# Performance work log

Measured on AMD Instinct MI355X. Metric: run time of the kernel, lower is better.

The kernel has to match this reference:

```python
import jax, jax.numpy as jnp
import numpy as np

B, S, D_IN, D_OUT, H = 4, 2048, 2048, 2048, 16
DH = D_OUT // H  # 128


def setup_inputs() -> dict:
    key = jax.random.key(0)
    ks = jax.random.split(key, 6)
    scale = 1.0 / np.sqrt(D_IN)
    return {
        "x": jax.random.normal(ks[0], (B, S, D_IN), dtype=jnp.float32),
        "Wq": jax.random.normal(ks[1], (D_IN, D_OUT), dtype=jnp.float32) * scale,
        "Wk": jax.random.normal(ks[2], (D_IN, D_OUT), dtype=jnp.float32) * scale,
        "Wv": jax.random.normal(ks[3], (D_IN, D_OUT), dtype=jnp.float32) * scale,
        "Wo": jax.random.normal(ks[4], (D_OUT, D_OUT), dtype=jnp.float32) * scale,
        "bo": jax.random.normal(ks[5], (D_OUT,), dtype=jnp.float32) * 0.01,
    }


def reference(x, Wq, Wk, Wv, Wo, bo):
    b, s, _ = x.shape
    # QKV projections (Linear, no bias), split into heads: [b, s, H, DH]
    q = (x @ Wq).reshape(b, s, H, DH)
    k = (x @ Wk).reshape(b, s, H, DH)
    v = (x @ Wv).reshape(b, s, H, DH)
    # attn_scores = Q @ K^T  -> [b, H, s, s]
    scores = jnp.einsum("bqhd,bkhd->bhqk", q, k)
    # causal mask: position q may only attend to k <= q
    causal = jnp.tril(jnp.ones((s, s), dtype=bool))
    scores = jnp.where(causal, scores, -jnp.inf)
    attn = jax.nn.softmax(scores / np.sqrt(DH).astype(np.float32), axis=-1)
    # dropout p = 0.0 -> identity
    ctx = jnp.einsum("bhqk,bkhd->bqhd", attn, v).reshape(b, s, D_OUT)
    return ctx @ Wo + bo
```

## Files before the change

### kernel.cpp

```cpp
#include <hip/hip_runtime.h>
#include <stdint.h>

typedef unsigned short u16;
typedef __attribute__((ext_vector_type(4))) float f32x4;
typedef __attribute__((ext_vector_type(8))) __bf16 bf16x8;
typedef __attribute__((address_space(3))) void lds_void;
typedef const __attribute__((address_space(1))) void gbl_void;

__device__ __forceinline__ u16 f2bf(float f) {
    uint32_t u = __float_as_uint(f);
    u += 0x7FFFu + ((u >> 16) & 1u);
    return (u16)(u >> 16);
}

__global__ __launch_bounds__(256) void cvt_bf16_kernel(const float* __restrict__ in,
                                                       u16* __restrict__ out, int n4) {
    int i = blockIdx.x * 256 + threadIdx.x;
    if (i >= n4) return;
    float4 v = reinterpret_cast<const float4*>(in)[i];
    ushort4 o;
    o.x = f2bf(v.x); o.y = f2bf(v.y); o.z = f2bf(v.z); o.w = f2bf(v.w);
    reinterpret_cast<ushort4*>(out)[i] = o;
}

__global__ __launch_bounds__(256) void transpose_w_kernel(const float* __restrict__ W,
                                                          u16* __restrict__ Wt) {
    __shared__ float tile[32][33];
    const int bx = blockIdx.x, by = blockIdx.y;
    const int tx = threadIdx.x;
    const int ty = threadIdx.y;
#pragma unroll
    for (int i = 0; i < 4; i++)
        tile[ty + i * 8][tx] = W[(size_t)(by * 32 + ty + i * 8) * 2048 + bx * 32 + tx];
    __syncthreads();
#pragma unroll
    for (int i = 0; i < 4; i++)
        Wt[(size_t)(bx * 32 + ty + i * 8) * 2048 + by * 32 + tx] = f2bf(tile[tx][ty + i * 8]);
}

template <bool F32OUT>
__global__ __launch_bounds__(256) void gemm_bt_kernel(const u16* __restrict__ A,
                                                      const u16* __restrict__ Bt,
                                                      void* __restrict__ Cout,
                                                      const float* __restrict__ bias,
                                                      int M, int N, int K) {
    __shared__ u16 As[3 * 4096];
    __shared__ u16 Bs[3 * 4096];
    const int tid = threadIdx.x;
    const int lane = tid & 63, wave = tid >> 6;
    const int l15 = lane & 15, l4 = lane >> 4;
    const int wm = wave >> 1, wn = wave & 1;

    const int gx = gridDim.x;
    const int nwg = gx * gridDim.y;
    const int flat0 = blockIdx.y * gx + blockIdx.x;
    const int q = nwg >> 3, r = nwg & 7;
    const int xcd = flat0 & 7, idx = flat0 >> 3;
    const int wgid = (xcd < r ? xcd * (q + 1) : r * (q + 1) + (xcd - r) * q) + idx;
    const int bm = wgid % gx, bn = wgid / gx;

    f32x4 acc[4][4] = {};

    const int r0 = tid >> 2;
    const int r1 = r0 + 64;
    const int c0 = (tid & 3) * 8;
    const u16* ga0 = A + (size_t)(bm * 128 + r0) * K + c0;
    const u16* ga1 = A + (size_t)(bm * 128 + r1) * K + c0;
    const u16* gb0 = Bt + (size_t)(bn * 128 + r0) * K + c0;
    const u16* gb1 = Bt + (size_t)(bn * 128 + r1) * K + c0;
    const int woff = wave * 1024;

#define STAGE_TILE(T, SLOT)                                                              \
    {                                                                                    \
        const int kb_ = (T) << 5;                                                        \
        const int sb_ = (SLOT) * 8192;                                                   \
        __builtin_amdgcn_global_load_lds((gbl_void*)(ga0 + kb_),                         \
                                         (lds_void*)((char*)As + sb_ + woff), 16, 0, 0); \
        __builtin_amdgcn_global_load_lds((gbl_void*)(ga1 + kb_),                         \
                                         (lds_void*)((char*)As + sb_ + 4096 + woff), 16, 0, 0); \
        __builtin_amdgcn_global_load_lds((gbl_void*)(gb0 + kb_),                         \
                                         (lds_void*)((char*)Bs + sb_ + woff), 16, 0, 0); \
        __builtin_amdgcn_global_load_lds((gbl_void*)(gb1 + kb_),                         \
                                         (lds_void*)((char*)Bs + sb_ + 4096 + woff), 16, 0, 0); \
    }

    const int nt = K >> 5;
    STAGE_TILE(0, 0);
    STAGE_TILE(1, 1);

    int cs = 0, ps = 2;
    for (int t = 0; t < nt; ++t) {
        if (t + 2 < nt) {
            STAGE_TILE(t + 2, ps);
            asm volatile("s_waitcnt vmcnt(8)" ::: "memory");
        } else if (t + 2 == nt) {
            asm volatile("s_waitcnt vmcnt(4)" ::: "memory");
        } else {
            asm volatile("s_waitcnt vmcnt(0)" ::: "memory");
        }
        __builtin_amdgcn_s_barrier();
        __builtin_amdgcn_sched_barrier(0);

        const u16* as = As + cs * 4096;
        const u16* bs = Bs + cs * 4096;
        bf16x8 af[4], bfr[4];
#pragma unroll
        for (int m = 0; m < 4; ++m)
            af[m] = *reinterpret_cast<const bf16x8*>(&as[(wm * 64 + m * 16 + l15) * 32 + l4 * 8]);
#pragma unroll
        for (int n = 0; n < 4; ++n)
            bfr[n] = *reinterpret_cast<const bf16x8*>(&bs[(wn * 64 + n * 16 + l15) * 32 + l4 * 8]);
#pragma unroll
        for (int m = 0; m < 4; ++m)
#pragma unroll
            for (int n = 0; n < 4; ++n)
                acc[m][n] = __builtin_amdgcn_mfma_f32_16x16x32_bf16(af[m], bfr[n], acc[m][n], 0, 0, 0);

        __builtin_amdgcn_s_barrier();
        __builtin_amdgcn_sched_barrier(0);
        cs = (cs == 2) ? 0 : cs + 1;
        ps = (ps == 2) ? 0 : ps + 1;
    }
#undef STAGE_TILE

    const int rbase = bm * 128 + wm * 64;
    const int cbase = bn * 128 + wn * 64;
#pragma unroll
    for (int m = 0; m < 4; ++m) {
#pragma unroll
        for (int n = 0; n < 4; ++n) {
            const int c = cbase + n * 16 + l15;
#pragma unroll
            for (int j = 0; j < 4; ++j) {
                const int rr = rbase + m * 16 + l4 * 4 + j;
                if (F32OUT)
                    ((float*)Cout)[(size_t)rr * N + c] = acc[m][n][j] + bias[c];
                else
                    ((u16*)Cout)[(size_t)rr * N + c] = f2bf(acc[m][n][j]);
            }
        }
    }
}

__global__ __launch_bounds__(256) void attn_kernel(const u16* __restrict__ qk,
                                                   const u16* __restrict__ vt,
                                                   u16* __restrict__ ctx) {
    __shared__ u16 Ks[64 * 128];
    __shared__ u16 Vs[128 * 64];
    __shared__ u16 Ps[4 * 16 * 64];
    const int tid = threadIdx.x, lane = tid & 63, w = tid >> 6;
    const int l15 = lane & 15, l4 = lane >> 4;
    const int flat = blockIdx.x;
    const int qt = 31 - (flat >> 6);
    const int bh = flat & 63;
    const int b = bh >> 4, h = bh & 15;
    const int qb = qt * 64;

    bf16x8 qf[4];
    {
        const size_t rowQ = (size_t)(b * 2048 + qb + w * 16 + l15) * 4096 + h * 128;
#pragma unroll
        for (int kk = 0; kk < 4; kk++)
            qf[kk] = *reinterpret_cast<const bf16x8*>(&qk[rowQ + kk * 32 + l4 * 8]);
    }

    const int krow_i = tid >> 4, kslot = tid & 15;
    const int vrow_i = tid >> 3, vslot = tid & 7;

    float m_r[4], l_r[4];
    f32x4 o[8] = {};
#pragma unroll
    for (int j = 0; j < 4; ++j) { m_r[j] = -1e30f; l_r[j] = 0.f; }

    for (int kt = 0; kt <= qt; ++kt) {
        const int kvb = kt * 64;
#pragma unroll
        for (int p = 0; p < 4; ++p) {
            const int rowk = p * 16 + krow_i;
            const int ck = kslot ^ (rowk & 15);
            __builtin_amdgcn_global_load_lds(
                (gbl_void*)(qk + (size_t)(b * 2048 + kvb + rowk) * 4096 + 2048 + h * 128 + ck * 8),
                (lds_void*)((char*)Ks + p * 4096 + w * 1024), 16, 0, 0);
        }
#pragma unroll
        for (int p = 0; p < 4; ++p) {
            const int rowv = p * 32 + vrow_i;
            const int cv = vslot ^ (rowv & 7);
            __builtin_amdgcn_global_load_lds(
                (gbl_void*)(vt + (size_t)(h * 128 + rowv) * 8192 + b * 2048 + kvb + cv * 8),
                (lds_void*)((char*)Vs + p * 4096 + w * 1024), 16, 0, 0);
        }
        __syncthreads();

        f32x4 s[4] = {};
#pragma unroll
        for (int cb = 0; cb < 4; ++cb) {
            const int krow = cb * 16 + l15;
#pragma unroll
            for (int kk = 0; kk < 4; ++kk) {
                bf16x8 kf = *reinterpret_cast<const bf16x8*>(
                    &Ks[krow * 128 + (((kk * 4 + l4) ^ (krow & 15)) << 3)]);
                s[cb] = __builtin_amdgcn_mfma_f32_16x16x32_bf16(qf[kk], kf, s[cb], 0, 0, 0);
            }
        }
        const float sc = 0.08838834764831845f;
#pragma unroll
        for (int cb = 0; cb < 4; ++cb) s[cb] *= sc;

        if (kt == qt) {
#pragma unroll
            for (int cb = 0; cb < 4; ++cb)
#pragma unroll
                for (int j = 0; j < 4; ++j) {
                    int lr = w * 16 + l4 * 4 + j, lc = cb * 16 + l15;
                    if (lc > lr) s[cb][j] = -1e30f;
                }
        }

#pragma unroll
        for (int j = 0; j < 4; ++j) {
            float tm = fmaxf(fmaxf(s[0][j], s[1][j]), fmaxf(s[2][j], s[3][j]));
#pragma unroll
            for (int msk = 1; msk < 16; msk <<= 1)
                tm = fmaxf(tm, __shfl_xor(tm, msk, 64));
            float mnew = fmaxf(m_r[j], tm);
            float alpha = __expf(m_r[j] - mnew);
            m_r[j] = mnew;
            float rs = 0.f;
#pragma unroll
            for (int cb = 0; cb < 4; ++cb) {
                float p = __expf(s[cb][j] - mnew);
                s[cb][j] = p;
                rs += p;
            }
#pragma unroll
            for (int msk = 1; msk < 16; msk <<= 1)
                rs += __shfl_xor(rs, msk, 64);
            l_r[j] = l_r[j] * alpha + rs;
#pragma unroll
            for (int d = 0; d < 8; ++d) o[d][j] *= alpha;
        }

#pragma unroll
        for (int cb = 0; cb < 4; ++cb)
#pragma unroll
            for (int j = 0; j < 4; ++j) {
                const int rr = l4 * 4 + j;
                const int e = cb * 16 + l15;
                Ps[w * 1024 + rr * 64 + (((e >> 3) ^ (rr & 7)) << 3) + (e & 7)] = f2bf(s[cb][j]);
            }

#pragma unroll
        for (int ks = 0; ks < 2; ++ks) {
            bf16x8 pf = *reinterpret_cast<const bf16x8*>(
                &Ps[w * 1024 + l15 * 64 + (((ks * 4 + l4) ^ (l15 & 7)) << 3)]);
#pragma unroll
            for (int d = 0; d < 8; ++d) {
                const int dr = d * 16 + l15;
                bf16x8 vf = *reinterpret_cast<const bf16x8*>(
                    &Vs[dr * 64 + (((ks * 4 + l4) ^ (dr & 7)) << 3)]);
                o[d] = __builtin_amdgcn_mfma_f32_16x16x32_bf16(pf, vf, o[d], 0, 0, 0);
            }
        }
        __syncthreads();
    }

#pragma unroll
    for (int j = 0; j < 4; ++j) {
        float inv = 1.0f / l_r[j];
        size_t row = (size_t)(b * 2048 + qb + w * 16 + l4 * 4 + j) * 2048 + h * 128;
#pragma unroll
        for (int d = 0; d < 8; ++d)
            ctx[row + d * 16 + l15] = f2bf(o[d][j] * inv);
    }
}

extern "C" void kernel_launch(void* const* d_in, const int* in_sizes, int n_in,
                              void* d_out, int out_size, void* d_ws, size_t ws_size,
                              hipStream_t stream) {
    const float* x  = (const float*)d_in[0];
    const float* Wq = (const float*)d_in[1];
    const float* Wk = (const float*)d_in[2];
    const float* Wv = (const float*)d_in[3];
    const float* Wo = (const float*)d_in[4];
    const float* bo = (const float*)d_in[5];
    float* out = (float*)d_out;

    char* ws = (char*)d_ws;
    u16* xb  = (u16*)(ws);
    u16* wt  = (u16*)(ws + 33554432);
    u16* wto = (u16*)(ws + 33554432 + 25165824);
    u16* qk  = (u16*)(ws + 67108864);
    u16* vtb = (u16*)(ws + 134217728);
    u16* wtv = wt + 2 * 2048 * 2048;
    u16* ctxb = xb;

    cvt_bf16_kernel<<<16384, 256, 0, stream>>>(x, xb, 4194304);
    dim3 tb(32, 8), tg(64, 64);
    transpose_w_kernel<<<tg, tb, 0, stream>>>(Wq, wt);
    transpose_w_kernel<<<tg, tb, 0, stream>>>(Wk, wt + 2048 * 2048);
    transpose_w_kernel<<<tg, tb, 0, stream>>>(Wv, wtv);
    transpose_w_kernel<<<tg, tb, 0, stream>>>(Wo, wto);

    gemm_bt_kernel<false><<<dim3(64, 32), 256, 0, stream>>>(xb, wt, qk, nullptr, 8192, 4096, 2048);
    gemm_bt_kernel<false><<<dim3(16, 64), 256, 0, stream>>>(wtv, xb, vtb, nullptr, 2048, 8192, 2048);
    attn_kernel<<<2048, 256, 0, stream>>>(qk, vtb, ctxb);
    gemm_bt_kernel<true><<<dim3(64, 16), 256, 0, stream>>>(ctxb, wto, out, bo, 8192, 2048, 2048);
}
```

Measured before the change: 590.2 us.

## Add 1024-thread 256x256-tile GEMM for QK projection and drop XCD remap

Adds a new GEMM kernel that uses 16 waves per workgroup and a 256x256 output tile, with a 64-wide K step. Operands are staged directly into XOR-swizzled LDS through global_load_lds, double-buffered, and each K step is split into four quadrant phases with barriers and setprio around the MFMAs. The QK projection now uses this kernel to get more operand reuse per byte loaded and fewer workgroups. Separately, the XCD-aware workgroup remapping in the existing 128x128 GEMM is removed in favour of plain blockIdx mapping, which may hurt L2 locality for the V and output GEMMs.

```diff
diff --git a/kernel.cpp b/kernel.cpp
--- a/kernel.cpp
+++ b/kernel.cpp
@@ -36,6 +36,121 @@
 #pragma unroll
     for (int i = 0; i < 4; i++)
         Wt[(size_t)(bx * 32 + ty + i * 8) * 2048 + by * 32 + tx] = f2bf(tile[tx][ty + i * 8]);
+}
+
+template <bool F32OUT>
+__global__ __launch_bounds__(1024) void gemm1024_kernel(const u16* __restrict__ A,
+                                                        const u16* __restrict__ Bt,
+                                                        void* __restrict__ Cout,
+                                                        const float* __restrict__ bias,
+                                                        int M, int N, int K) {
+    __shared__ u16 lds[65536];
+    const int tid = threadIdx.x;
+    const int lane = tid & 63, w = tid >> 6;
+    const int l15 = lane & 15, l4 = lane >> 4;
+    const int wm2 = w >> 2, wn2 = w & 3;
+    const int bm = blockIdx.x, bn = blockIdx.y;
+
+    f32x4 acc[4][4] = {};
+
+    const int srow = tid >> 3;
+    const int scs = (tid & 7) ^ (srow & 7);
+    const u16* gA = A + (size_t)(bm * 256 + srow) * K + scs * 8;
+    const u16* gB = Bt + (size_t)(bn * 256 + srow) * K + scs * 8;
+    const size_t rowK128 = (size_t)128 * K;
+    u16* ldst = lds + tid * 8;
+
+#define STAGE_HALF(D, OP, H, T)                                                     \
+    __builtin_amdgcn_global_load_lds(                                               \
+        (gbl_void*)(((OP) ? gB : gA) + (size_t)(H) * rowK128 + (size_t)(T) * 64),   \
+        (lds_void*)(ldst + (D) * 32768 + (OP) * 16384 + (H) * 8192), 16, 0, 0);
+
+#define PHASE(D, Q, T1, ST, GEND)                                                   \
+    {                                                                               \
+        if ((Q) == 0 && (ST)) {                                                     \
+            STAGE_HALF((D) ^ 1, 0, 0, T1);                                          \
+            STAGE_HALF((D) ^ 1, 0, 1, T1);                                          \
+            STAGE_HALF((D) ^ 1, 1, 0, T1);                                          \
+            STAGE_HALF((D) ^ 1, 1, 1, T1);                                          \
+        }                                                                           \
+        const int mh = (Q) >> 1, nh = (Q) & 1;                                      \
+        bf16x8 af[2][2], bfr[2][2];                                                 \
+        _Pragma("unroll") for (int mm = 0; mm < 2; ++mm) {                          \
+            const int ra = wm2 * 64 + mh * 32 + mm * 16 + l15;                      \
+            _Pragma("unroll") for (int kk = 0; kk < 2; ++kk)                        \
+                af[mm][kk] = *reinterpret_cast<const bf16x8*>(                      \
+                    &lds[(D) * 32768 + ra * 64 + (((kk * 4 + l4) ^ (ra & 7)) << 3)]);\
+        }                                                                           \
+        _Pragma("unroll") for (int nn = 0; nn < 2; ++nn) {                          \
+            const int rb = wn2 * 64 + nh * 32 + nn * 16 + l15;                      \
+            _Pragma("unroll") for (int kk = 0; kk < 2; ++kk)                        \
+                bfr[nn][kk] = *reinterpret_cast<const bf16x8*>(                     \
+                    &lds[(D) * 32768 + 16384 + rb * 64 +                            \
+                         (((kk * 4 + l4) ^ (rb & 7)) << 3)]);                       \
+        }                                                                           \
+        __builtin_amdgcn_s_barrier();                                               \
+        asm volatile("s_waitcnt lgkmcnt(0)" ::: "memory");                          \
+        __builtin_amdgcn_sched_barrier(0);                                          \
+        __builtin_amdgcn_s_setprio(1);                                              \
+        _Pragma("unroll") for (int kk = 0; kk < 2; ++kk)                            \
+            _Pragma("unroll") for (int mm = 0; mm < 2; ++mm)                        \
+                _Pragma("unroll") for (int nn = 0; nn < 2; ++nn)                    \
+                    acc[mh * 2 + mm][nh * 2 + nn] =                                 \
+                        __builtin_amdgcn_mfma_f32_16x16x32_bf16(                    \
+                            af[mm][kk], bfr[nn][kk], acc[mh * 2 + mm][nh * 2 + nn], \
+                            0, 0, 0);                                               \
+        __builtin_amdgcn_s_setprio(0);                                              \
+        if (GEND) {                                                                 \
+            asm volatile("s_waitcnt vmcnt(0)" ::: "memory");                        \
+            __builtin_amdgcn_sched_barrier(0);                                      \
+        }                                                                           \
+        __builtin_amdgcn_s_barrier();                                               \
+        __builtin_amdgcn_sched_barrier(0);                                          \
+    }
+
+    const int nt = K >> 6;
+    STAGE_HALF(0, 0, 0, 0);
+    STAGE_HALF(0, 0, 1, 0);
+    STAGE_HALF(0, 1, 0, 0);
+    STAGE_HALF(0, 1, 1, 0);
+    asm volatile("s_waitcnt vmcnt(0)" ::: "memory");
+    __builtin_amdgcn_sched_barrier(0);
+    __builtin_amdgcn_s_barrier();
+
+    for (int T = 0; T < nt; ++T) {
+        const bool st = (T + 1 < nt);
+        if ((T & 1) == 0) {
+            PHASE(0, 0, T + 1, st, false);
+            PHASE(0, 1, T + 1, st, false);
+            PHASE(0, 2, T + 1, st, false);
+            PHASE(0, 3, T + 1, st, true);
+        } else {
+            PHASE(1, 0, T + 1, st, false);
+            PHASE(1, 1, T + 1, st, false);
+            PHASE(1, 2, T + 1, st, false);
+            PHASE(1, 3, T + 1, st, true);
+        }
+    }
+#undef PHASE
+#undef STAGE_HALF
+
+    const int rbase = bm * 256 + wm2 * 64;
+    const int cbase = bn * 256 + wn2 * 64;
+#pragma unroll
+    for (int mi = 0; mi < 4; ++mi) {
+#pragma unroll
+        for (int ni = 0; ni < 4; ++ni) {
+            const int c = cbase + ni * 16 + l15;
+#pragma unroll
+            for (int j = 0; j < 4; ++j) {
+                const int rr = rbase + mi * 16 + l4 * 4 + j;
+                if (F32OUT)
+                    ((float*)Cout)[(size_t)rr * N + c] = acc[mi][ni][j] + bias[c];
+                else
+                    ((u16*)Cout)[(size_t)rr * N + c] = f2bf(acc[mi][ni][j]);
+            }
+        }
+    }
 }
 
 template <bool F32OUT>
@@ -50,14 +165,7 @@
     const int lane = tid & 63, wave = tid >> 6;
     const int l15 = lane & 15, l4 = lane >> 4;
     const int wm = wave >> 1, wn = wave & 1;
-
-    const int gx = gridDim.x;
-    const int nwg = gx * gridDim.y;
-    const int flat0 = blockIdx.y * gx + blockIdx.x;
-    const int q = nwg >> 3, r = nwg & 7;
-    const int xcd = flat0 & 7, idx = flat0 >> 3;
-    const int wgid = (xcd < r ? xcd * (q + 1) : r * (q + 1) + (xcd - r) * q) + idx;
-    const int bm = wgid % gx, bn = wgid / gx;
+    const int bm = blockIdx.x, bn = blockIdx.y;
 
     f32x4 acc[4][4] = {};
 
@@ -302,7 +410,7 @@
     transpose_w_kernel<<<tg, tb, 0, stream>>>(Wv, wtv);
     transpose_w_kernel<<<tg, tb, 0, stream>>>(Wo, wto);
 
-    gemm_bt_kernel<false><<<dim3(64, 32), 256, 0, stream>>>(xb, wt, qk, nullptr, 8192, 4096, 2048);
+    gemm1024_kernel<false><<<dim3(32, 16), 1024, 0, stream>>>(xb, wt, qk, nullptr, 8192, 4096, 2048);
     gemm_bt_kernel<false><<<dim3(16, 64), 256, 0, stream>>>(wtv, xb, vtb, nullptr, 2048, 8192, 2048);
     attn_kernel<<<2048, 256, 0, stream>>>(qk, vtb, ctxb);
     gemm_bt_kernel<true><<<dim3(64, 16), 256, 0, stream>>>(ctxb, wto, out, bo, 8192, 2048, 2048);
```

New measurement: 1.476 ms. 2.5x slower.

## Double-buffer K/V tiles in attention kernel with async global-to-LDS prefetch

Applied to the files above, without the earlier changes.

Adds a second LDS buffer for the K and V tiles and issues the next tile's global_load_lds before computing on the current one. Partial vmcnt waits and raw s_barriers replace the full __syncthreads, so memory latency can overlap the QK^T and PV MFMAs. This doubles K/V LDS use (about 72KB per block), which may reduce occupancy. Correctness depends on the hand-counted vmcnt(8) and on the barrier placement.

```diff
diff --git a/kernel.cpp b/kernel.cpp
--- a/kernel.cpp
+++ b/kernel.cpp
@@ -145,8 +145,8 @@
 __global__ __launch_bounds__(256) void attn_kernel(const u16* __restrict__ qk,
                                                    const u16* __restrict__ vt,
                                                    u16* __restrict__ ctx) {
-    __shared__ u16 Ks[64 * 128];
-    __shared__ u16 Vs[128 * 64];
+    __shared__ u16 Ks[2 * 64 * 128];
+    __shared__ u16 Vs[2 * 128 * 64];
     __shared__ u16 Ps[4 * 16 * 64];
     const int tid = threadIdx.x, lane = tid & 63, w = tid >> 6;
     const int l15 = lane & 15, l4 = lane >> 4;
@@ -167,30 +167,45 @@
     const int krow_i = tid >> 4, kslot = tid & 15;
     const int vrow_i = tid >> 3, vslot = tid & 7;
 
+#define STAGE_KV(BUF, KT)                                                                \
+    {                                                                                    \
+        const int kvb_ = (KT) * 64;                                                      \
+        _Pragma("unroll") for (int p = 0; p < 4; ++p) {                                  \
+            const int rowk = p * 16 + krow_i;                                            \
+            const int ck = kslot ^ (rowk & 15);                                          \
+            __builtin_amdgcn_global_load_lds(                                            \
+                (gbl_void*)(qk + (size_t)(b * 2048 + kvb_ + rowk) * 4096 + 2048 +        \
+                            h * 128 + ck * 8),                                           \
+                (lds_void*)((char*)Ks + (BUF) * 16384 + p * 4096 + w * 1024), 16, 0, 0); \
+        }                                                                                \
+        _Pragma("unroll") for (int p = 0; p < 4; ++p) {                                  \
+            const int rowv = p * 32 + vrow_i;                                            \
+            const int cv = vslot ^ (rowv & 7);                                           \
+            __builtin_amdgcn_global_load_lds(                                            \
+                (gbl_void*)(vt + (size_t)(h * 128 + rowv) * 8192 + b * 2048 + kvb_ +     \
+                            cv * 8),                                                     \
+                (lds_void*)((char*)Vs + (BUF) * 16384 + p * 4096 + w * 1024), 16, 0, 0); \
+        }                                                                                \
+    }
+
     float m_r[4], l_r[4];
     f32x4 o[8] = {};
 #pragma unroll
     for (int j = 0; j < 4; ++j) { m_r[j] = -1e30f; l_r[j] = 0.f; }
 
+    STAGE_KV(0, 0);
+
     for (int kt = 0; kt <= qt; ++kt) {
-        const int kvb = kt * 64;
-#pragma unroll
-        for (int p = 0; p < 4; ++p) {
-            const int rowk = p * 16 + krow_i;
-            const int ck = kslot ^ (rowk & 15);
-            __builtin_amdgcn_global_load_lds(
-                (gbl_void*)(qk + (size_t)(b * 2048 + kvb + rowk) * 4096 + 2048 + h * 128 + ck * 8),
-                (lds_void*)((char*)Ks + p * 4096 + w * 1024), 16, 0, 0);
-        }
-#pragma unroll
-        for (int p = 0; p < 4; ++p) {
-            const int rowv = p * 32 + vrow_i;
-            const int cv = vslot ^ (rowv & 7);
-            __builtin_amdgcn_global_load_lds(
-                (gbl_void*)(vt + (size_t)(h * 128 + rowv) * 8192 + b * 2048 + kvb + cv * 8),
-                (lds_void*)((char*)Vs + p * 4096 + w * 1024), 16, 0, 0);
-        }
-        __syncthreads();
+        const int buf = kt & 1;
+        const int kb16 = buf * 8192;
+        if (kt < qt) {
+            STAGE_KV(buf ^ 1, kt + 1);
+            asm volatile("s_waitcnt vmcnt(8)" ::: "memory");
+        } else {
+            asm volatile("s_waitcnt vmcnt(0)" ::: "memory");
+        }
+        __builtin_amdgcn_s_barrier();
+        __builtin_amdgcn_sched_barrier(0);
 
         f32x4 s[4] = {};
 #pragma unroll
@@ -199,7 +214,7 @@
 #pragma unroll
             for (int kk = 0; kk < 4; ++kk) {
                 bf16x8 kf = *reinterpret_cast<const bf16x8*>(
-                    &Ks[krow * 128 + (((kk * 4 + l4) ^ (krow & 15)) << 3)]);
+                    &Ks[kb16 + krow * 128 + (((kk * 4 + l4) ^ (krow & 15)) << 3)]);
                 s[cb] = __builtin_amdgcn_mfma_f32_16x16x32_bf16(qf[kk], kf, s[cb], 0, 0, 0);
             }
         }
@@ -258,12 +273,14 @@
             for (int d = 0; d < 8; ++d) {
                 const int dr = d * 16 + l15;
                 bf16x8 vf = *reinterpret_cast<const bf16x8*>(
-                    &Vs[dr * 64 + (((ks * 4 + l4) ^ (dr & 7)) << 3)]);
+                    &Vs[kb16 + dr * 64 + (((ks * 4 + l4) ^ (dr & 7)) << 3)]);
                 o[d] = __builtin_amdgcn_mfma_f32_16x16x32_bf16(pf, vf, o[d], 0, 0, 0);
             }
         }
-        __syncthreads();
-    }
+        __builtin_amdgcn_s_barrier();
+        __builtin_amdgcn_sched_barrier(0);
+    }
+#undef STAGE_KV
 
 #pragma unroll
     for (int j = 0; j < 4; ++j) {
```

New measurement: 599.5 us. Within noise of the previous version (+1.6%).
